# Kernel optimization log

Measured on AMD Instinct MI355X. Metric: run time of the kernel, lower is better.

Reference implementation:

```python
import jax, jax.numpy as jnp
import numpy as np
from jax import lax

T = 64
TAU = 2.0
ALPHA = 4.0  # spikingjelly surrogate.Sigmoid default
V_TH = 1.0

@jax.custom_vjp
def spike(v):
    # Heaviside(v) with sigmoid surrogate gradient
    return (v >= 0.0).astype(v.dtype)

def _spike_fwd(v):
    return spike(v), v

def _spike_bwd(v, g):
    s = jax.nn.sigmoid(ALPHA * v)
    return (g * ALPHA * s * (1.0 - s),)

spike.defvjp(_spike_fwd, _spike_bwd)

def setup_inputs() -> dict:
    key = jax.random.key(0)
    k1, k2, k3 = jax.random.split(key, 3)
    x = jax.random.normal(k1, (2048, 28, 28), dtype=jnp.float32)
    W1 = jax.random.normal(k2, (1024, 784), dtype=jnp.float32) * (1.0 / np.sqrt(784))
    W2 = jax.random.normal(k3, (10, 1024), dtype=jnp.float32) * (1.0 / np.sqrt(1024))
    return {"x": x, "W1": W1, "W2": W2}

def _lif_step(v, c):
    # decay_input=True: v += (x - (v - v_reset)) / tau, v_reset = 0
    v = v + (c - v) / TAU
    s = spike(v - V_TH)
    v = v * (1.0 - s)  # hard reset to 0
    return v, s

def reference(x, W1, W2):
    B = x.shape[0]
    xf = x.reshape(B, -1)                      # [B, 784]
    c1 = xf @ W1.T                              # [B, 1024], identical every timestep
    v1_0 = jnp.zeros((B, W1.shape[0]), x.dtype)
    v2_0 = jnp.zeros((B, W2.shape[0]), x.dtype)

    def step(carry, _):
        v1, v2 = carry
        v1, s1 = _lif_step(v1, c1)              # [B, 1024]
        c2 = s1 @ W2.T                          # [B, 10]
        v2, s2 = _lif_step(v2, c2)              # [B, 10]
        return (v1, v2), s2

    _, out = lax.scan(step, (v1_0, v2_0), None, length=T)
    return out  # [T, B, 10]
```

## Files before the change

### kernel.cpp

```cpp
#include <hip/hip_runtime.h>
#include <stdint.h>

typedef unsigned long long u64;
typedef unsigned int u32;

#define T_STEPS 64
#define KDIM 784
#define N1 1024
#define NB 2048
#define N2 10

__global__ void k_w2t(const float* __restrict__ W2, float* __restrict__ W2T) {
    int j = blockIdx.x * blockDim.x + threadIdx.x;
    if (j >= N1) return;
    float r[12];
#pragma unroll
    for (int i = 0; i < 10; ++i) r[i] = W2[i * N1 + j];
    r[10] = 0.f; r[11] = 0.f;
#pragma unroll
    for (int i = 0; i < 12; ++i) W2T[j * 12 + i] = r[i];
}

__global__ __launch_bounds__(256) void k_transpose2(
    const float* __restrict__ X, float* __restrict__ Xt,
    const float* __restrict__ W1, float* __restrict__ W1t)
{
    __shared__ float t[32][33];
    int b = blockIdx.x;
    const float* src; float* dst; int R;
    int tile_r, tile_c;
    if (b < 1600) { src = X;  dst = Xt;  R = NB; tile_r = b / 25; tile_c = b % 25; }
    else { b -= 1600; src = W1; dst = W1t; R = N1; tile_r = b / 25; tile_c = b % 25; }

    const int tx = threadIdx.x & 31, ty = threadIdx.x >> 5;
    const int r0 = tile_r << 5, c0 = tile_c << 5;

#pragma unroll
    for (int i = 0; i < 32; i += 8) {
        int c = c0 + tx;
        t[ty + i][tx] = (c < KDIM) ? src[(size_t)(r0 + ty + i) * KDIM + c] : 0.f;
    }
    __syncthreads();
#pragma unroll
    for (int i = 0; i < 32; i += 8) {
        int c = c0 + ty + i;
        if (c < KDIM) dst[(size_t)c * R + r0 + tx] = t[tx][ty + i];
    }
}

#define NSTEP (KDIM / 16)

typedef const __attribute__((address_space(1))) void gas_void;
typedef __attribute__((address_space(3))) void las_void;

__global__ __launch_bounds__(256) void k_gemm_lif1(
    const float* __restrict__ Xt,
    const float* __restrict__ W1t,
    u64* __restrict__ bits)
{
    __shared__ __align__(16) float A2[2][16][64];
    __shared__ __align__(16) float B2[2][16][64];

    const int tid  = threadIdx.x;
    const int lane = tid & 63;
    const int tx   = tid & 15;
    const int ty   = tid >> 4;
    const int bm   = blockIdx.y << 6;
    const int bn   = blockIdx.x << 6;

    const int w4   = __builtin_amdgcn_readfirstlane((tid >> 6) << 2);
    const int srow = w4 + (lane >> 4);
    const int scol = (lane & 15) << 2;

    const float* gA = Xt  + (size_t)srow * NB + bm + scol;
    const float* gB = W1t + (size_t)srow * N1 + bn + scol;

#define STAGE(pp, t)                                                          \
    {                                                                         \
        __builtin_amdgcn_global_load_lds((gas_void*)(gA + (size_t)(t) * (16 * NB)), \
                                         (las_void*)&A2[pp][w4][0], 16, 0, 0); \
        __builtin_amdgcn_global_load_lds((gas_void*)(gB + (size_t)(t) * (16 * N1)), \
                                         (las_void*)&B2[pp][w4][0], 16, 0, 0); \
    }

    float acc[4][4];
#pragma unroll
    for (int r = 0; r < 4; ++r)
#pragma unroll
        for (int c = 0; c < 4; ++c) acc[r][c] = 0.f;

    STAGE(0, 0);
    asm volatile("s_waitcnt vmcnt(0)" ::: "memory");
    __builtin_amdgcn_s_barrier();
    __builtin_amdgcn_sched_barrier(0);

    int p = 0;
    for (int t = 0; t < NSTEP; ++t) {
        if (t + 1 < NSTEP) STAGE(p ^ 1, t + 1);
#pragma unroll
        for (int kk = 0; kk < 16; ++kk) {
            float4 av = *(const float4*)(&A2[p][kk][ty << 2]);
            float4 bv = *(const float4*)(&B2[p][kk][tx << 2]);
            acc[0][0] = fmaf(av.x, bv.x, acc[0][0]); acc[0][1] = fmaf(av.x, bv.y, acc[0][1]);
            acc[0][2] = fmaf(av.x, bv.z, acc[0][2]); acc[0][3] = fmaf(av.x, bv.w, acc[0][3]);
            acc[1][0] = fmaf(av.y, bv.x, acc[1][0]); acc[1][1] = fmaf(av.y, bv.y, acc[1][1]);
            acc[1][2] = fmaf(av.y, bv.z, acc[1][2]); acc[1][3] = fmaf(av.y, bv.w, acc[1][3]);
            acc[2][0] = fmaf(av.z, bv.x, acc[2][0]); acc[2][1] = fmaf(av.z, bv.y, acc[2][1]);
            acc[2][2] = fmaf(av.z, bv.z, acc[2][2]); acc[2][3] = fmaf(av.z, bv.w, acc[2][3]);
            acc[3][0] = fmaf(av.w, bv.x, acc[3][0]); acc[3][1] = fmaf(av.w, bv.y, acc[3][1]);
            acc[3][2] = fmaf(av.w, bv.z, acc[3][2]); acc[3][3] = fmaf(av.w, bv.w, acc[3][3]);
        }
        asm volatile("s_waitcnt vmcnt(0)" ::: "memory");
        __builtin_amdgcn_s_barrier();
        __builtin_amdgcn_sched_barrier(0);
        p ^= 1;
    }
#undef STAGE

    float c[16], v[16];
    u32 blo[16], bhi[16];
#pragma unroll
    for (int u = 0; u < 16; ++u) {
        c[u] = acc[u >> 2][u & 3];
        v[u] = 0.f; blo[u] = 0u; bhi[u] = 0u;
    }
    for (int t = 0; t < 32; ++t) {
#pragma unroll
        for (int u = 0; u < 16; ++u) {
            v[u] += (c[u] - v[u]) * 0.5f;
            bool s = v[u] >= 1.0f;
            blo[u] |= (s ? 1u : 0u) << t;
            v[u] = s ? 0.f : v[u];
        }
    }
    for (int t = 0; t < 32; ++t) {
#pragma unroll
        for (int u = 0; u < 16; ++u) {
            v[u] += (c[u] - v[u]) * 0.5f;
            bool s = v[u] >= 1.0f;
            bhi[u] |= (s ? 1u : 0u) << t;
            v[u] = s ? 0.f : v[u];
        }
    }
#pragma unroll
    for (int u = 0; u < 16; ++u) {
        int r = u >> 2, cc = u & 3;
        bits[(size_t)(bm + (ty << 2) + r) * N1 + (bn + (tx << 2) + cc)] =
            ((u64)bhi[u] << 32) | (u64)blo[u];
    }
}

__global__ __launch_bounds__(256) void k_lif2(
    const u64* __restrict__ bits, const float* __restrict__ W2T,
    float* __restrict__ out)
{
    __shared__ u64  masksS[N1];
    __shared__ u32  idxS[N1];
    __shared__ float c2S[4][64][12];
    __shared__ float s2S[64][10];

    const int tid  = threadIdx.x;
    const int w    = tid >> 6;
    const int lane = tid & 63;
    const int b    = blockIdx.x;

    const u64* row = bits + (size_t)b * N1;
    const int base_j = w << 8;

    int nact = 0;
#pragma unroll
    for (int it = 0; it < 4; ++it) {
        int j = base_j + (it << 6) + lane;
        u64 m = row[j];
        u64 ball = __ballot(m != 0ULL);
        int pos = nact + __popcll(ball & ((1ULL << lane) - 1ULL));
        if (m != 0ULL) { masksS[base_j + pos] = m; idxS[base_j + pos] = j; }
        nact += __popcll(ball);
    }

    float acc[10];
#pragma unroll
    for (int i = 0; i < 10; ++i) acc[i] = 0.f;

#define LIF2_BODY(A)                                                      \
    {                                                                     \
        u64 m = masksS[(A)];                                              \
        int j = __builtin_amdgcn_readfirstlane((int)idxS[(A)]);           \
        float sf = (float)((m >> lane) & 1ULL);                           \
        const float* wr = W2T + j * 12;                                   \
        float4 w0 = *(const float4*)(wr);                                 \
        float4 w1 = *(const float4*)(wr + 4);                             \
        float2 w2 = *(const float2*)(wr + 8);                             \
        acc[0] += sf * w0.x; acc[1] += sf * w0.y;                         \
        acc[2] += sf * w0.z; acc[3] += sf * w0.w;                         \
        acc[4] += sf * w1.x; acc[5] += sf * w1.y;                         \
        acc[6] += sf * w1.z; acc[7] += sf * w1.w;                         \
        acc[8] += sf * w2.x; acc[9] += sf * w2.y;                         \
    }

    int a = 0;
    for (; a + 2 <= nact; a += 2) { LIF2_BODY(base_j + a); LIF2_BODY(base_j + a + 1); }
    if (a < nact) LIF2_BODY(base_j + a);
#undef LIF2_BODY

#pragma unroll
    for (int i = 0; i < 10; ++i) c2S[w][lane][i] = acc[i];
    __syncthreads();

    if (tid < 10) {
        const int i = tid;
        float v2 = 0.f;
        for (int t = 0; t < 64; ++t) {
            float cc = ((c2S[0][t][i] + c2S[1][t][i]) + c2S[2][t][i]) + c2S[3][t][i];
            v2 += (cc - v2) * 0.5f;
            bool s = v2 >= 1.0f;
            s2S[t][i] = s ? 1.f : 0.f;
            v2 = s ? 0.f : v2;
        }
    }
    __syncthreads();

    for (int idx = tid; idx < 64 * 10; idx += 256) {
        int t = idx / 10, i = idx % 10;
        out[(size_t)t * (NB * N2) + (size_t)b * N2 + i] = s2S[t][i];
    }
}

extern "C" void kernel_launch(void* const* d_in, const int* in_sizes, int n_in,
                              void* d_out, int out_size, void* d_ws, size_t ws_size,
                              hipStream_t stream) {
    const float* X  = (const float*)d_in[0];
    const float* W1 = (const float*)d_in[1];
    const float* W2 = (const float*)d_in[2];
    float* out = (float*)d_out;

    char* ws = (char*)d_ws;
    u64*   bits = (u64*)ws;
    float* W2T  = (float*)(ws + (size_t)NB * N1 * 8);
    float* Xt   = (float*)(ws + (size_t)NB * N1 * 8 + 65536);
    float* W1t  = Xt + (size_t)KDIM * NB;

    k_w2t<<<dim3((N1 + 255) / 256), dim3(256), 0, stream>>>(W2, W2T);
    k_transpose2<<<dim3(2400), dim3(256), 0, stream>>>(X, Xt, W1, W1t);

    dim3 g1(N1 / 64, NB / 64);
    k_gemm_lif1<<<g1, dim3(256), 0, stream>>>(Xt, W1t, bits);

    k_lif2<<<dim3(NB), dim3(256), 0, stream>>>(bits, W2T, out);
}
```

Before: 164.2 us.

## Double GEMM block threads to 512 and batch sparse LIF2 loop by eight

The GEMM+LIF1 kernel now runs 512 threads per block, each computing a 2x4 instead of a 4x4 output tile. The first half of the threads stages A and the second half stages B into LDS. This is meant to expose more parallelism and hide latency in the LIF time loop, at the cost of lower register-level reuse per FMA. The LIF2 sparse accumulation loop now pads the active-mask list to a multiple of eight with zero masks and processes eight entries per iteration to overlap the W2T loads.

After: 191.2 us. +16.4%, slower.

```diff
diff --git a/kernel.cpp b/kernel.cpp
--- a/kernel.cpp
+++ b/kernel.cpp
@@ -53,7 +53,7 @@
 typedef const __attribute__((address_space(1))) void gas_void;
 typedef __attribute__((address_space(3))) void las_void;
 
-__global__ __launch_bounds__(256) void k_gemm_lif1(
+__global__ __launch_bounds__(512) void k_gemm_lif1(
     const float* __restrict__ Xt,
     const float* __restrict__ W1t,
     u64* __restrict__ bits)
@@ -64,28 +64,31 @@
     const int tid  = threadIdx.x;
     const int lane = tid & 63;
     const int tx   = tid & 15;
-    const int ty   = tid >> 4;
+    const int tyy  = tid >> 4;
     const int bm   = blockIdx.y << 6;
     const int bn   = blockIdx.x << 6;
 
-    const int w4   = __builtin_amdgcn_readfirstlane((tid >> 6) << 2);
+    const int stid = (tid < 256) ? tid : tid - 256;
+    const int w4   = __builtin_amdgcn_readfirstlane((stid >> 6) << 2);
     const int srow = w4 + (lane >> 4);
     const int scol = (lane & 15) << 2;
 
     const float* gA = Xt  + (size_t)srow * NB + bm + scol;
     const float* gB = W1t + (size_t)srow * N1 + bn + scol;
 
-#define STAGE(pp, t)                                                          \
-    {                                                                         \
-        __builtin_amdgcn_global_load_lds((gas_void*)(gA + (size_t)(t) * (16 * NB)), \
-                                         (las_void*)&A2[pp][w4][0], 16, 0, 0); \
-        __builtin_amdgcn_global_load_lds((gas_void*)(gB + (size_t)(t) * (16 * N1)), \
-                                         (las_void*)&B2[pp][w4][0], 16, 0, 0); \
-    }
-
-    float acc[4][4];
-#pragma unroll
-    for (int r = 0; r < 4; ++r)
+#define STAGE(pp, t)                                                              \
+    {                                                                             \
+        if (tid < 256)                                                            \
+            __builtin_amdgcn_global_load_lds((gas_void*)(gA + (size_t)(t) * (16 * NB)), \
+                                             (las_void*)&A2[pp][w4][0], 16, 0, 0); \
+        else                                                                      \
+            __builtin_amdgcn_global_load_lds((gas_void*)(gB + (size_t)(t) * (16 * N1)), \
+                                             (las_void*)&B2[pp][w4][0], 16, 0, 0); \
+    }
+
+    float acc[2][4];
+#pragma unroll
+    for (int r = 0; r < 2; ++r)
 #pragma unroll
         for (int c = 0; c < 4; ++c) acc[r][c] = 0.f;
 
@@ -99,16 +102,12 @@
         if (t + 1 < NSTEP) STAGE(p ^ 1, t + 1);
 #pragma unroll
         for (int kk = 0; kk < 16; ++kk) {
-            float4 av = *(const float4*)(&A2[p][kk][ty << 2]);
+            float2 av = *(const float2*)(&A2[p][kk][tyy << 1]);
             float4 bv = *(const float4*)(&B2[p][kk][tx << 2]);
             acc[0][0] = fmaf(av.x, bv.x, acc[0][0]); acc[0][1] = fmaf(av.x, bv.y, acc[0][1]);
             acc[0][2] = fmaf(av.x, bv.z, acc[0][2]); acc[0][3] = fmaf(av.x, bv.w, acc[0][3]);
             acc[1][0] = fmaf(av.y, bv.x, acc[1][0]); acc[1][1] = fmaf(av.y, bv.y, acc[1][1]);
             acc[1][2] = fmaf(av.y, bv.z, acc[1][2]); acc[1][3] = fmaf(av.y, bv.w, acc[1][3]);
-            acc[2][0] = fmaf(av.z, bv.x, acc[2][0]); acc[2][1] = fmaf(av.z, bv.y, acc[2][1]);
-            acc[2][2] = fmaf(av.z, bv.z, acc[2][2]); acc[2][3] = fmaf(av.z, bv.w, acc[2][3]);
-            acc[3][0] = fmaf(av.w, bv.x, acc[3][0]); acc[3][1] = fmaf(av.w, bv.y, acc[3][1]);
-            acc[3][2] = fmaf(av.w, bv.z, acc[3][2]); acc[3][3] = fmaf(av.w, bv.w, acc[3][3]);
         }
         asm volatile("s_waitcnt vmcnt(0)" ::: "memory");
         __builtin_amdgcn_s_barrier();
@@ -117,16 +116,16 @@
     }
 #undef STAGE
 
-    float c[16], v[16];
-    u32 blo[16], bhi[16];
-#pragma unroll
-    for (int u = 0; u < 16; ++u) {
+    float c[8], v[8];
+    u32 blo[8], bhi[8];
+#pragma unroll
+    for (int u = 0; u < 8; ++u) {
         c[u] = acc[u >> 2][u & 3];
         v[u] = 0.f; blo[u] = 0u; bhi[u] = 0u;
     }
     for (int t = 0; t < 32; ++t) {
 #pragma unroll
-        for (int u = 0; u < 16; ++u) {
+        for (int u = 0; u < 8; ++u) {
             v[u] += (c[u] - v[u]) * 0.5f;
             bool s = v[u] >= 1.0f;
             blo[u] |= (s ? 1u : 0u) << t;
@@ -135,7 +134,7 @@
     }
     for (int t = 0; t < 32; ++t) {
 #pragma unroll
-        for (int u = 0; u < 16; ++u) {
+        for (int u = 0; u < 8; ++u) {
             v[u] += (c[u] - v[u]) * 0.5f;
             bool s = v[u] >= 1.0f;
             bhi[u] |= (s ? 1u : 0u) << t;
@@ -143,9 +142,9 @@
         }
     }
 #pragma unroll
-    for (int u = 0; u < 16; ++u) {
+    for (int u = 0; u < 8; ++u) {
         int r = u >> 2, cc = u & 3;
-        bits[(size_t)(bm + (ty << 2) + r) * N1 + (bn + (tx << 2) + cc)] =
+        bits[(size_t)(bm + (tyy << 1) + r) * N1 + (bn + (tx << 2) + cc)] =
             ((u64)bhi[u] << 32) | (u64)blo[u];
     }
 }
@@ -177,31 +176,34 @@
         if (m != 0ULL) { masksS[base_j + pos] = m; idxS[base_j + pos] = j; }
         nact += __popcll(ball);
     }
+    const int npad = (nact + 7) & ~7;
+    if (lane < npad - nact) { masksS[base_j + nact + lane] = 0ULL; idxS[base_j + nact + lane] = 0u; }
 
     float acc[10];
 #pragma unroll
     for (int i = 0; i < 10; ++i) acc[i] = 0.f;
 
-#define LIF2_BODY(A)                                                      \
-    {                                                                     \
-        u64 m = masksS[(A)];                                              \
-        int j = __builtin_amdgcn_readfirstlane((int)idxS[(A)]);           \
-        float sf = (float)((m >> lane) & 1ULL);                           \
-        const float* wr = W2T + j * 12;                                   \
-        float4 w0 = *(const float4*)(wr);                                 \
-        float4 w1 = *(const float4*)(wr + 4);                             \
-        float2 w2 = *(const float2*)(wr + 8);                             \
-        acc[0] += sf * w0.x; acc[1] += sf * w0.y;                         \
-        acc[2] += sf * w0.z; acc[3] += sf * w0.w;                         \
-        acc[4] += sf * w1.x; acc[5] += sf * w1.y;                         \
-        acc[6] += sf * w1.z; acc[7] += sf * w1.w;                         \
-        acc[8] += sf * w2.x; acc[9] += sf * w2.y;                         \
-    }
-
-    int a = 0;
-    for (; a + 2 <= nact; a += 2) { LIF2_BODY(base_j + a); LIF2_BODY(base_j + a + 1); }
-    if (a < nact) LIF2_BODY(base_j + a);
-#undef LIF2_BODY
+    for (int a = 0; a < npad; a += 8) {
+        u64 m[8]; u32 j[8];
+#pragma unroll
+        for (int q = 0; q < 8; ++q) {
+            m[q] = masksS[base_j + a + q];
+            j[q] = idxS[base_j + a + q];
+        }
+#pragma unroll
+        for (int q = 0; q < 8; ++q) {
+            float sf = (float)((m[q] >> lane) & 1ULL);
+            const float* wr = W2T + j[q] * 12;
+            float4 w0 = *(const float4*)(wr);
+            float4 w1 = *(const float4*)(wr + 4);
+            float2 w2 = *(const float2*)(wr + 8);
+            acc[0] = fmaf(sf, w0.x, acc[0]); acc[1] = fmaf(sf, w0.y, acc[1]);
+            acc[2] = fmaf(sf, w0.z, acc[2]); acc[3] = fmaf(sf, w0.w, acc[3]);
+            acc[4] = fmaf(sf, w1.x, acc[4]); acc[5] = fmaf(sf, w1.y, acc[5]);
+            acc[6] = fmaf(sf, w1.z, acc[6]); acc[7] = fmaf(sf, w1.w, acc[7]);
+            acc[8] = fmaf(sf, w2.x, acc[8]); acc[9] = fmaf(sf, w2.y, acc[9]);
+        }
+    }
 
 #pragma unroll
     for (int i = 0; i < 10; ++i) c2S[w][lane][i] = acc[i];
@@ -244,7 +246,7 @@
     k_transpose2<<<dim3(2400), dim3(256), 0, stream>>>(X, Xt, W1, W1t);
 
     dim3 g1(N1 / 64, NB / 64);
-    k_gemm_lif1<<<g1, dim3(256), 0, stream>>>(Xt, W1t, bits);
+    k_gemm_lif1<<<g1, dim3(512), 0, stream>>>(Xt, W1t, bits);
 
     k_lif2<<<dim3(NB), dim3(256), 0, stream>>>(bits, W2T, out);
 }
```
